# Performance work log

Measured on AMD Instinct MI355X. Metric: run time of the kernel, lower is better.

Reference implementation:

```python
import jax, jax.numpy as jnp
import numpy as np

B, LQ, E = 4, 8400, 256
HEADS, LEVELS, POINTS = 8, 4, 4
HEAD_DIM = E // HEADS
SHAPES = [(80, 80), (40, 40), (20, 20), (10, 10)]  # (H, W) per level; sum HW = 8400
LV = sum(h * w for h, w in SHAPES)


def setup_inputs() -> dict:
    key = jax.random.key(0)
    ks = jax.random.split(key, 12)
    query = jax.random.normal(ks[0], (B, LQ, E), jnp.float32)
    # per-level normalized reference points in (0.1, 0.9)
    reference_points = 0.1 + 0.8 * jax.random.uniform(ks[1], (B, LQ, LEVELS, 2), jnp.float32)
    value = jax.random.normal(ks[2], (B, LV, E), jnp.float32)
    spatial_shapes = jnp.array(SHAPES, dtype=jnp.int32)
    s = 0.05
    Wv = jax.random.normal(ks[3], (E, E), jnp.float32) * s
    bv = jnp.zeros((E,), jnp.float32)
    Woff = jax.random.normal(ks[4], (E, HEADS * LEVELS * POINTS * 2), jnp.float32) * 0.01
    boff = jax.random.normal(ks[5], (HEADS * LEVELS * POINTS * 2,), jnp.float32) * 0.02
    Wattn = jax.random.normal(ks[6], (E, HEADS * LEVELS * POINTS), jnp.float32) * s
    battn = jnp.zeros((HEADS * LEVELS * POINTS,), jnp.float32)
    Wo = jax.random.normal(ks[7], (E, E), jnp.float32) * s
    bo = jnp.zeros((E,), jnp.float32)
    return dict(query=query, reference_points=reference_points, value=value,
                spatial_shapes=spatial_shapes, Wv=Wv, bv=bv, Woff=Woff, boff=boff,
                Wattn=Wattn, battn=battn, Wo=Wo, bo=bo)


def _bilinear_sample(vflat, x, y, Hl, Wl):
    # vflat: [BH, D, Hl*Wl]; x, y: [BH, N] pixel coords (align_corners=False convention)
    x0f = jnp.floor(x); y0f = jnp.floor(y)
    wx = (x - x0f)[:, None, :]; wy = (y - y0f)[:, None, :]
    x0 = x0f.astype(jnp.int32); y0 = y0f.astype(jnp.int32)

    def gather(ix, iy):
        valid = ((ix >= 0) & (ix < Wl) & (iy >= 0) & (iy < Hl)).astype(vflat.dtype)
        idx = jnp.clip(iy, 0, Hl - 1) * Wl + jnp.clip(ix, 0, Wl - 1)
        g = jnp.take_along_axis(vflat, idx[:, None, :], axis=2)  # [BH, D, N]
        return g * valid[:, None, :]

    v00 = gather(x0, y0); v01 = gather(x0 + 1, y0)
    v10 = gather(x0, y0 + 1); v11 = gather(x0 + 1, y0 + 1)
    return (v00 * (1 - wx) * (1 - wy) + v01 * wx * (1 - wy)
            + v10 * (1 - wx) * wy + v11 * wx * wy)


def _msda_forward(query, reference_points, value, spatial_shapes,
                  Wv, bv, Woff, boff, Wattn, battn, Wo, bo):
    b, lq, _ = query.shape
    v = (value @ Wv + bv).reshape(b, -1, HEADS, HEAD_DIM)
    off = (query @ Woff + boff).reshape(b, lq, HEADS, LEVELS, POINTS, 2)
    aw = (query @ Wattn + battn).reshape(b, lq, HEADS, LEVELS * POINTS)
    aw = jax.nn.softmax(aw, axis=-1).reshape(b, lq, HEADS, LEVELS, POINTS)
    # normalizer (W, H) per level
    norm = jnp.stack([spatial_shapes[:, 1], spatial_shapes[:, 0]], axis=-1).astype(query.dtype)
    # sampling locations in [0,1]: [B, Lq, H, L, P, 2]
    loc = reference_points[:, :, None, :, None, :] + off / norm[None, None, None, :, None, :]

    sampled_levels = []
    start = 0
    for lvl, (Hl, Wl) in enumerate(SHAPES):
        vl = v[:, start:start + Hl * Wl]                      # [B, Hl*Wl, H, D]
        start += Hl * Wl
        vflat = vl.transpose(0, 2, 3, 1).reshape(b * HEADS, HEAD_DIM, Hl * Wl)
        grid = loc[:, :, :, lvl]                              # [B, Lq, H, P, 2]
        grid = grid.transpose(0, 2, 1, 3, 4).reshape(b * HEADS, lq * POINTS, 2)
        g = grid * 2.0 - 1.0                                  # grid_sample convention
        x = (g[..., 0] + 1.0) * (Wl * 0.5) - 0.5
        y = (g[..., 1] + 1.0) * (Hl * 0.5) - 0.5
        s = _bilinear_sample(vflat, x, y, Hl, Wl)             # [BH, D, Lq*P]
        sampled_levels.append(s.reshape(b, HEADS, HEAD_DIM, lq, POINTS))
    sampled = jnp.stack(sampled_levels, axis=-1)              # [B, H, D, Lq, P, L]
    out = jnp.einsum('bhdqpl,bqhlp->bqhd', sampled, aw).reshape(b, lq, E)
    return out @ Wo + bo


def reference(query, reference_points, value, spatial_shapes,
              Wv, bv, Woff, boff, Wattn, battn, Wo, bo):
    return _msda_forward(query, reference_points, value, spatial_shapes,
                         Wv, bv, Woff, boff, Wattn, battn, Wo, bo)
```

## Files before the change

### kernel.cpp

```cpp
#include <hip/hip_runtime.h>
#include <math.h>

#define BB 4
#define LQ 8400
#define NH 8
#define LVTOT 8500
#define HD 32
#define PLANE_USH 544000

typedef __attribute__((ext_vector_type(8))) short short8;
typedef __attribute__((ext_vector_type(4))) float f32x4;
typedef __attribute__((ext_vector_type(2))) _Float16 half2_t;
typedef __attribute__((ext_vector_type(2))) __fp16 fp16x2_t;
typedef unsigned short ushort_t;

__device__ __forceinline__ ushort_t f2bf(float f) {
    union { float f; unsigned u; } v; v.f = f;
    unsigned r = v.u + 0x7fffu + ((v.u >> 16) & 1u);
    return (ushort_t)(r >> 16);
}
__device__ __forceinline__ float bflo(unsigned u) {
    union { unsigned u; float f; } x; x.u = u << 16; return x.f;
}
__device__ __forceinline__ float bfhi(unsigned u) {
    union { unsigned u; float f; } x; x.u = u & 0xffff0000u; return x.f;
}
__device__ __forceinline__ half2_t ash2(unsigned u) {
    union { unsigned u; half2_t h; } x; x.u = u; return x.h;
}
__device__ __forceinline__ unsigned pk2u(fp16x2_t h) {
    union { fp16x2_t h; unsigned u; } x; x.h = h; return x.u;
}

__device__ __forceinline__ void dma16(const ushort_t* g, ushort_t* l) {
    __builtin_amdgcn_global_load_lds(
        (const __attribute__((address_space(1))) void*)g,
        (__attribute__((address_space(3))) void*)l, 16, 0, 0);
}

__device__ __forceinline__ void lvl_decomp(int pix, int& lb, int& y, int& x,
                                           int& rowp) {
    if (pix < 6400)      { y = pix / 80;            x = pix - y * 80;  rowp = 40; lb = 0; }
    else if (pix < 8000) { int r = pix - 6400; y = r / 40; x = r - y * 40; rowp = 20; lb = 3200; }
    else if (pix < 8400) { int r = pix - 8000; y = r / 20; x = r - y * 20; rowp = 10; lb = 4000; }
    else                 { int r = pix - 8400; y = r / 10; x = r - y * 10; rowp = 5;  lb = 4200; }
}

__global__ __launch_bounds__(256) void prep_all(
    const float* __restrict__ value, const float* __restrict__ query,
    const float* __restrict__ Wv, const float* __restrict__ Woff,
    const float* __restrict__ Wattn, const float* __restrict__ Wo,
    ushort_t* __restrict__ value_b, ushort_t* __restrict__ query_b,
    ushort_t* __restrict__ BT)
{
    const int bid = blockIdx.x;
    if (bid < 16900) {
        const float* src = (bid < 8500) ? value : query;
        ushort_t* dst = (bid < 8500) ? value_b : query_b;
        int i = (bid < 8500 ? bid : bid - 8500) * 256 + threadIdx.x;
        float4 f = ((const float4*)src)[i];
        ushort4 o;
        o.x = f2bf(f.x); o.y = f2bf(f.y); o.z = f2bf(f.z); o.w = f2bf(f.w);
        ((ushort4*)dst)[i] = o;
    } else {
        int idx = (bid - 16900) * 256 + threadIdx.x;
        int r = idx >> 8, k = idx & 255;
        float v;
        if (r < 256) v = Wv[k * 256 + r];
        else if (r < 640) {
            int n = r - 256;
            v = (n < 256) ? Woff[k * 256 + n] : Wattn[k * 128 + (n - 256)];
        } else v = Wo[k * 256 + (r - 640)];
        BT[idx] = f2bf(v);
    }
}

__device__ __forceinline__ void gemm_core(
    const ushort_t* __restrict__ A, const ushort_t* __restrict__ B, int M,
    int m0, int n0, ushort_t* Asl, ushort_t* Bsl, f32x4 acc[4][4])
{
    const int tid  = threadIdx.x;
    const int wave = tid >> 6, lane = tid & 63;
    const int quad = lane >> 4, mr = lane & 15;
    const int wm   = (wave >> 1) * 64, wn = (wave & 1) * 64;
    const int oct  = lane >> 3;
    const int bseg = lane & 7;

    for (int k0 = 0; k0 < 256; k0 += 64) {
        __syncthreads();
        #pragma unroll
        for (int i = 0; i < 4; i++) {
            int m  = i * 32 + wave * 8 + oct;
            int gs = bseg ^ (m & 7);
            int am = min(m0 + m, M - 1);
            dma16(A + (size_t)am * 256 + k0 + gs * 8,
                  Asl + (size_t)(i * 32 + wave * 8) * 64 + lane * 8);
            int bn = n0 + m;
            dma16(B + (size_t)bn * 256 + k0 + gs * 8,
                  Bsl + (size_t)(i * 32 + wave * 8) * 64 + lane * 8);
        }
        __syncthreads();
        #pragma unroll
        for (int ks = 0; ks < 2; ks++) {
            short8 af[4], bf[4];
            const int ksl = ks * 4 + quad;
            #pragma unroll
            for (int i = 0; i < 4; i++) {
                int m = wm + i * 16 + mr;
                af[i] = *(const short8*)&Asl[m * 64 + (ksl ^ (m & 7)) * 8];
                int n = wn + i * 16 + mr;
                bf[i] = *(const short8*)&Bsl[n * 64 + (ksl ^ (n & 7)) * 8];
            }
            #pragma unroll
            for (int i = 0; i < 4; i++)
                #pragma unroll
                for (int j = 0; j < 4; j++)
                    acc[i][j] = __builtin_amdgcn_mfma_f32_16x16x32_bf16(
                        af[i], bf[j], acc[i][j], 0, 0, 0);
        }
    }
}

__global__ __launch_bounds__(256, 3) void gemm_fused(
    const ushort_t* __restrict__ Av, const ushort_t* __restrict__ Aq,
    const ushort_t* __restrict__ BT,
    const float* __restrict__ bv, const float* __restrict__ boff,
    const float* __restrict__ battn,
    ushort_t* __restrict__ vperm, ushort_t* __restrict__ off_b,
    ushort_t* __restrict__ awl_b)
{
    __shared__ ushort_t smem[16384];
    ushort_t* Asl = smem;
    ushort_t* Bsl = smem + 8192;

    const int bid = blockIdx.x;
    int mode, m0, n0, M;
    const ushort_t *A, *B;
    if (bid < 532) { mode = 0; m0 = (bid >> 1) * 128; n0 = (bid & 1) * 128;
                     A = Av; B = BT; M = 34000; }
    else { int b2 = bid - 532;
           mode = 1; m0 = (b2 / 3) * 128; n0 = (b2 % 3) * 128;
           A = Aq; B = BT + 65536; M = 33600; }

    f32x4 acc[4][4];
    #pragma unroll
    for (int i = 0; i < 4; i++)
        #pragma unroll
        for (int j = 0; j < 4; j++) acc[i][j] = (f32x4){0.f, 0.f, 0.f, 0.f};

    gemm_core(A, B, M, m0, n0, Asl, Bsl, acc);

    const int tid  = threadIdx.x;
    const int wave = tid >> 6, lane = tid & 63;
    const int quad = lane >> 4, mr = lane & 15;
    const int wm   = (wave >> 1) * 64, wn = (wave & 1) * 64;

    __syncthreads();
    #pragma unroll
    for (int i = 0; i < 4; i++) {
        #pragma unroll
        for (int j = 0; j < 4; j++) {
            const int lc = wn + j * 16 + mr;
            const int c  = n0 + lc;
            const float bias = (mode == 0) ? bv[c]
                              : (c < 256 ? boff[c] : battn[c - 256]);
            #pragma unroll
            for (int reg = 0; reg < 4; reg++) {
                const int rl = wm + i * 16 + quad * 4 + reg;
                float val = acc[i][j][reg] + bias;
                ushort_t u;
                if (mode == 0) { union { _Float16 h; ushort_t u; } cv;
                                 cv.h = (_Float16)val; u = cv.u; }
                else u = f2bf(val);
                smem[rl * 128 + (lc ^ ((rl & 3) << 3))] = u;
            }
        }
    }
    __syncthreads();

    if (mode == 1) {
        for (int k = 0; k < 8; k++) {
            int sid = k * 256 + tid;
            int rl = sid >> 4, cc = (sid & 15) * 8;
            int row = m0 + rl;
            if (row >= M) continue;
            uint4 v = *(const uint4*)&smem[rl * 128 + (cc ^ ((rl & 3) << 3))];
            if (n0 < 256) *(uint4*)&off_b[(size_t)row * 256 + n0 + cc] = v;
            else          *(uint4*)&awl_b[(size_t)row * 128 + cc] = v;
        }
    } else {
        const int hb = n0 >> 5;
        for (int k = 0; k < 16; k++) {
            int sid = k * 256 + tid;
            int unit = sid >> 5;
            if (unit >= 127) continue;
            int sub = sid & 31;
            int hh = sub >> 3, q = sub & 7;
            int copy = (unit >= 64) ? 1 : 0;
            int t = copy ? ((unit - 64) * 2 + 1) : (unit * 2);
            int row = m0 + t;
            if (row + 1 >= 34000) continue;
            int b = row / LVTOT, pix = row - b * LVTOT;
            int lb, y, x, rowp;
            lvl_decomp(pix, lb, y, x, rowp);
            if (copy && x >= 2 * rowp - 1) continue;
            int p = x >> 1;
            int pidx = copy * 4250 + lb + y * rowp + p;
            int h = hb + hh;
            uint2 a  = *(const uint2*)&smem[t * 128 +
                          ((hh * 32 + q * 4) ^ ((t & 3) << 3))];
            uint2 b2 = *(const uint2*)&smem[(t + 1) * 128 +
                          ((hh * 32 + q * 4) ^ (((t + 1) & 3) << 3))];
            uint4 o;
            o.x = (a.x & 0xffffu) | (b2.x << 16);
            o.y = (a.x >> 16)     | (b2.x & 0xffff0000u);
            o.z = (a.y & 0xffffu) | (b2.y << 16);
            o.w = (a.y >> 16)     | (b2.y & 0xffff0000u);
            *(uint4*)((char*)(vperm + (size_t)(b * NH + h) * PLANE_USH)
                      + (size_t)pidx * 128 + q * 16) = o;
        }
        {
            int pixsel = tid >> 7;
            int rem = tid & 127;
            int hh = rem >> 5, d = rem & 31;
            int t = pixsel ? 127 : 0;
            int row = m0 + t;
            if (row < 34000) {
                int b = row / LVTOT, pix = row - b * LVTOT;
                int lb, y, x, rowp;
                lvl_decomp(pix, lb, y, x, rowp);
                bool doit; int p, slot;
                if (!pixsel) { doit = (x >= 2);            p = (x - 2) >> 1; slot = 1; }
                else         { doit = (x < 2 * rowp - 1);  p = (x - 1) >> 1; slot = 0; }
                if (doit) {
                    int pidx = 4250 + lb + y * rowp + p;
                    int h = hb + hh;
                    vperm[(size_t)(b * NH + h) * PLANE_USH
                          + (size_t)pidx * 64 + d * 2 + slot] =
                        smem[t * 128 + ((hh * 32 + d) ^ ((t & 3) << 3))];
                }
            }
        }
    }
}

__global__ __launch_bounds__(256, 3) void gemm_out(
    const ushort_t* __restrict__ A, const ushort_t* __restrict__ BT,
    const float* __restrict__ bo, float* __restrict__ out)
{
    __shared__ ushort_t Asl[128 * 64];
    __shared__ ushort_t Bsl[128 * 64];

    const int m0 = (blockIdx.x >> 1) * 128;
    const int n0 = (blockIdx.x & 1) * 128;
    const int M = 33600;

    f32x4 acc[4][4];
    #pragma unroll
    for (int i = 0; i < 4; i++)
        #pragma unroll
        for (int j = 0; j < 4; j++) acc[i][j] = (f32x4){0.f, 0.f, 0.f, 0.f};

    gemm_core(A, BT, M, m0, n0, Asl, Bsl, acc);

    const int tid  = threadIdx.x;
    const int wave = tid >> 6, lane = tid & 63;
    const int quad = lane >> 4, mr = lane & 15;
    const int wm   = (wave >> 1) * 64, wn = (wave & 1) * 64;

    #pragma unroll
    for (int i = 0; i < 4; i++) {
        const int rbase = m0 + wm + i * 16 + quad * 4;
        #pragma unroll
        for (int j = 0; j < 4; j++) {
            const int c = n0 + wn + j * 16 + mr;
            #pragma unroll
            for (int reg = 0; reg < 4; reg++) {
                int row = rbase + reg;
                if (row >= M) continue;
                out[(size_t)row * 256 + c] = acc[i][j][reg] + bo[c];
            }
        }
    }
}

__global__ __launch_bounds__(256) void msda_sample(
    const ushort_t* __restrict__ vperm, const ushort_t* __restrict__ off,
    const ushort_t* __restrict__ awl, const float* __restrict__ refp,
    ushort_t* __restrict__ sampled)
{
    __shared__ int4 s_wi[16 * 33];

    const int tid = threadIdx.x;
    const int bid = blockIdx.x;
    const int h   = bid & 7;
    const int r   = bid >> 3;
    const int b   = r / 263;
    const int c   = r - b * 263;
    const int q0b = c * 32;
    const size_t bq0 = (size_t)b * LQ + q0b;

    const int Hs[4]    = {80, 40, 20, 10};
    const int pbase[4] = {0, 3200, 4000, 4200};

    #pragma unroll
    for (int it = 0; it < 2; it++) {
        const int s  = it * 256 + tid;
        const int ql = s >> 4, lp = s & 15;
        const int l  = lp >> 2;
        const int qv = (q0b + ql < LQ) ? ql : 0;
        const size_t bq = bq0 + qv;
        const int Wl = Hs[l];

        unsigned od = *(const unsigned*)(off + bq * 256 + h * 32 + lp * 2);
        float ox = bflo(od), oy = bfhi(od);
        float lgt = bflo((unsigned)awl[bq * 128 + h * 16 + lp]);
        float e = __expf(lgt);
        float sum = e;
        sum += __shfl_xor(sum, 1, 16);
        sum += __shfl_xor(sum, 2, 16);
        sum += __shfl_xor(sum, 4, 16);
        sum += __shfl_xor(sum, 8, 16);
        float aw = e * __builtin_amdgcn_rcpf(sum);

        float2 rp = *(const float2*)(refp + bq * 8 + l * 2);
        float x = rp.x * (float)Wl + ox - 0.5f;
        float y = rp.y * (float)Wl + oy - 0.5f;
        float x0f = floorf(x), y0f = floorf(y);
        float wx = x - x0f, wy = y - y0f;
        int x0 = (int)x0f, y0 = (int)y0f;
        float hx0 = ((x0 >= 0) & (x0 < Wl)) ? (1.f - wx) : 0.f;
        float hx1 = ((x0 + 1 >= 0) & (x0 + 1 < Wl)) ? wx : 0.f;
        float vy0w = ((y0 >= 0) & (y0 < Wl)) ? (1.f - wy) * aw : 0.f;
        float vy1w = ((y0 + 1 >= 0) & (y0 + 1 < Wl)) ? wy * aw : 0.f;
        int px = min(max(x0, 0), Wl - 2);
        float pl, pr;
        if (x0 < px)      { pl = hx1; pr = 0.f; }
        else if (x0 > px) { pl = 0.f; pr = hx0; }
        else              { pl = hx0; pr = hx1; }
        int cy0 = min(max(y0, 0), Wl - 1);
        int cy1 = min(max(y0 + 1, 0), Wl - 1);
        const int copy = px & 1;
        const int p    = copy ? ((px - 1) >> 1) : (px >> 1);
        const int rowp = Wl >> 1;
        const int cb   = copy * 4250 + pbase[l] + p;
        const int otop = (cb + cy0 * rowp) << 7;
        const int obot = (cb + cy1 * rowp) << 7;
        unsigned wt = pk2u(__builtin_amdgcn_cvt_pkrtz(pl * vy0w, pr * vy0w));
        unsigned wb = pk2u(__builtin_amdgcn_cvt_pkrtz(pl * vy1w, pr * vy1w));
        s_wi[lp * 33 + ql] = make_int4((int)wt, (int)wb, otop, obot);
    }
    __syncthreads();

    const int ql  = tid >> 3;
    const int l8  = tid & 7;
    const int dby = l8 * 16;

    if (q0b + ql < LQ) {
        const char* plane = (const char*)(vperm + (size_t)(b * NH + h) * PLANE_USH);
        float a0 = 0.f, a1 = 0.f, a2 = 0.f, a3 = 0.f;
        #pragma unroll
        for (int pt = 0; pt < 16; pt++) {
            int4 wi = s_wi[pt * 33 + ql];
            uint4 vt = *(const uint4*)(plane + (unsigned)(wi.z + dby));
            uint4 vb = *(const uint4*)(plane + (unsigned)(wi.w + dby));
            half2_t wt = ash2((unsigned)wi.x);
            half2_t wb = ash2((unsigned)wi.y);
            a0 = __builtin_amdgcn_fdot2(wt, ash2(vt.x), a0, false);
            a0 = __builtin_amdgcn_fdot2(wb, ash2(vb.x), a0, false);
            a1 = __builtin_amdgcn_fdot2(wt, ash2(vt.y), a1, false);
            a1 = __builtin_amdgcn_fdot2(wb, ash2(vb.y), a1, false);
            a2 = __builtin_amdgcn_fdot2(wt, ash2(vt.z), a2, false);
            a2 = __builtin_amdgcn_fdot2(wb, ash2(vb.z), a2, false);
            a3 = __builtin_amdgcn_fdot2(wt, ash2(vt.w), a3, false);
            a3 = __builtin_amdgcn_fdot2(wb, ash2(vb.w), a3, false);
        }
        const size_t bq = bq0 + ql;
        ushort4 o;
        o.x = f2bf(a0); o.y = f2bf(a1);
        o.z = f2bf(a2); o.w = f2bf(a3);
        *(ushort4*)(sampled + bq * 256 + h * 32 + l8 * 4) = o;
    }
}

extern "C" void kernel_launch(void* const* d_in, const int* in_sizes, int n_in,
                              void* d_out, int out_size, void* d_ws, size_t ws_size,
                              hipStream_t stream) {
    const float* query = (const float*)d_in[0];
    const float* refp  = (const float*)d_in[1];
    const float* value = (const float*)d_in[2];
    const float* Wv    = (const float*)d_in[4];
    const float* bv    = (const float*)d_in[5];
    const float* Woff  = (const float*)d_in[6];
    const float* boff  = (const float*)d_in[7];
    const float* Wattn = (const float*)d_in[8];
    const float* battn = (const float*)d_in[9];
    const float* Wo    = (const float*)d_in[10];
    const float* bo    = (const float*)d_in[11];
    float* out = (float*)d_out;

    ushort_t* ws = (ushort_t*)d_ws;
    ushort_t* off_b   = ws;
    ushort_t* awl_b   = off_b + 8601600;
    ushort_t* value_b = awl_b + 4300800;
    ushort_t* query_b = value_b + 8704000;
    ushort_t* vperm_b = query_b + 8601600;
    ushort_t* BT      = vperm_b + 17408000;
    ushort_t* sampled_b = query_b;

    prep_all<<<dim3(17796), 256, 0, stream>>>(
        value, query, Wv, Woff, Wattn, Wo, value_b, query_b, BT);

    gemm_fused<<<dim3(532 + 789), 256, 0, stream>>>(
        value_b, query_b, BT, bv, boff, battn, vperm_b, off_b, awl_b);

    msda_sample<<<dim3(8 * 4 * 263), 256, 0, stream>>>(
        vperm_b, off_b, awl_b, refp, sampled_b);

    gemm_out<<<dim3(526), 256, 0, stream>>>(
        sampled_b, BT + 163840, bo, out);
}
```

Before: 217.8 us.

## Enlarge GEMM tiles to 256x128 with 512-thread blocks

```diff
diff --git a/kernel.cpp b/kernel.cpp
--- a/kernel.cpp
+++ b/kernel.cpp
@@ -75,7 +75,7 @@
     }
 }
 
-__device__ __forceinline__ void gemm_core(
+__device__ __forceinline__ void gemm_core256(
     const ushort_t* __restrict__ A, const ushort_t* __restrict__ B, int M,
     int m0, int n0, ushort_t* Asl, ushort_t* Bsl, f32x4 acc[4][4])
 {
@@ -90,14 +90,19 @@
         __syncthreads();
         #pragma unroll
         for (int i = 0; i < 4; i++) {
-            int m  = i * 32 + wave * 8 + oct;
+            int m  = i * 64 + wave * 8 + oct;
             int gs = bseg ^ (m & 7);
             int am = min(m0 + m, M - 1);
             dma16(A + (size_t)am * 256 + k0 + gs * 8,
-                  Asl + (size_t)(i * 32 + wave * 8) * 64 + lane * 8);
-            int bn = n0 + m;
+                  Asl + (i * 64 + wave * 8) * 64 + lane * 8);
+        }
+        #pragma unroll
+        for (int i = 0; i < 2; i++) {
+            int n  = i * 64 + wave * 8 + oct;
+            int gs = bseg ^ (n & 7);
+            int bn = n0 + n;
             dma16(B + (size_t)bn * 256 + k0 + gs * 8,
-                  Bsl + (size_t)(i * 32 + wave * 8) * 64 + lane * 8);
+                  Bsl + (i * 64 + wave * 8) * 64 + lane * 8);
         }
         __syncthreads();
         #pragma unroll
@@ -121,7 +126,7 @@
     }
 }
 
-__global__ __launch_bounds__(256, 3) void gemm_fused(
+__global__ __launch_bounds__(512, 4) void gemm_fused(
     const ushort_t* __restrict__ Av, const ushort_t* __restrict__ Aq,
     const ushort_t* __restrict__ BT,
     const float* __restrict__ bv, const float* __restrict__ boff,
@@ -129,17 +134,17 @@
     ushort_t* __restrict__ vperm, ushort_t* __restrict__ off_b,
     ushort_t* __restrict__ awl_b)
 {
-    __shared__ ushort_t smem[16384];
+    __shared__ ushort_t smem[24576];
     ushort_t* Asl = smem;
-    ushort_t* Bsl = smem + 8192;
+    ushort_t* Bsl = smem + 16384;
 
     const int bid = blockIdx.x;
     int mode, m0, n0, M;
     const ushort_t *A, *B;
-    if (bid < 532) { mode = 0; m0 = (bid >> 1) * 128; n0 = (bid & 1) * 128;
+    if (bid < 266) { mode = 0; m0 = (bid >> 1) * 256; n0 = (bid & 1) * 128;
                      A = Av; B = BT; M = 34000; }
-    else { int b2 = bid - 532;
-           mode = 1; m0 = (b2 / 3) * 128; n0 = (b2 % 3) * 128;
+    else { int b2 = bid - 266;
+           mode = 1; m0 = (b2 / 3) * 256; n0 = (b2 % 3) * 128;
            A = Aq; B = BT + 65536; M = 33600; }
 
     f32x4 acc[4][4];
@@ -148,110 +153,120 @@
         #pragma unroll
         for (int j = 0; j < 4; j++) acc[i][j] = (f32x4){0.f, 0.f, 0.f, 0.f};
 
-    gemm_core(A, B, M, m0, n0, Asl, Bsl, acc);
+    gemm_core256(A, B, M, m0, n0, Asl, Bsl, acc);
 
     const int tid  = threadIdx.x;
     const int wave = tid >> 6, lane = tid & 63;
     const int quad = lane >> 4, mr = lane & 15;
     const int wm   = (wave >> 1) * 64, wn = (wave & 1) * 64;
+    const int whalf = wave >> 2;
 
     __syncthreads();
-    #pragma unroll
-    for (int i = 0; i < 4; i++) {
-        #pragma unroll
-        for (int j = 0; j < 4; j++) {
-            const int lc = wn + j * 16 + mr;
-            const int c  = n0 + lc;
-            const float bias = (mode == 0) ? bv[c]
-                              : (c < 256 ? boff[c] : battn[c - 256]);
-            #pragma unroll
-            for (int reg = 0; reg < 4; reg++) {
-                const int rl = wm + i * 16 + quad * 4 + reg;
-                float val = acc[i][j][reg] + bias;
-                ushort_t u;
-                if (mode == 0) { union { _Float16 h; ushort_t u; } cv;
-                                 cv.h = (_Float16)val; u = cv.u; }
-                else u = f2bf(val);
-                smem[rl * 128 + (lc ^ ((rl & 3) << 3))] = u;
-            }
-        }
-    }
-    __syncthreads();
-
-    if (mode == 1) {
-        for (int k = 0; k < 8; k++) {
-            int sid = k * 256 + tid;
-            int rl = sid >> 4, cc = (sid & 15) * 8;
-            int row = m0 + rl;
-            if (row >= M) continue;
-            uint4 v = *(const uint4*)&smem[rl * 128 + (cc ^ ((rl & 3) << 3))];
-            if (n0 < 256) *(uint4*)&off_b[(size_t)row * 256 + n0 + cc] = v;
-            else          *(uint4*)&awl_b[(size_t)row * 128 + cc] = v;
-        }
-    } else {
-        const int hb = n0 >> 5;
-        for (int k = 0; k < 16; k++) {
-            int sid = k * 256 + tid;
-            int unit = sid >> 5;
-            if (unit >= 127) continue;
-            int sub = sid & 31;
-            int hh = sub >> 3, q = sub & 7;
-            int copy = (unit >= 64) ? 1 : 0;
-            int t = copy ? ((unit - 64) * 2 + 1) : (unit * 2);
-            int row = m0 + t;
-            if (row + 1 >= 34000) continue;
-            int b = row / LVTOT, pix = row - b * LVTOT;
-            int lb, y, x, rowp;
-            lvl_decomp(pix, lb, y, x, rowp);
-            if (copy && x >= 2 * rowp - 1) continue;
-            int p = x >> 1;
-            int pidx = copy * 4250 + lb + y * rowp + p;
-            int h = hb + hh;
-            uint2 a  = *(const uint2*)&smem[t * 128 +
-                          ((hh * 32 + q * 4) ^ ((t & 3) << 3))];
-            uint2 b2 = *(const uint2*)&smem[(t + 1) * 128 +
-                          ((hh * 32 + q * 4) ^ (((t + 1) & 3) << 3))];
-            uint4 o;
-            o.x = (a.x & 0xffffu) | (b2.x << 16);
-            o.y = (a.x >> 16)     | (b2.x & 0xffff0000u);
-            o.z = (a.y & 0xffffu) | (b2.y << 16);
-            o.w = (a.y >> 16)     | (b2.y & 0xffff0000u);
-            *(uint4*)((char*)(vperm + (size_t)(b * NH + h) * PLANE_USH)
-                      + (size_t)pidx * 128 + q * 16) = o;
-        }
-        {
-            int pixsel = tid >> 7;
-            int rem = tid & 127;
-            int hh = rem >> 5, d = rem & 31;
-            int t = pixsel ? 127 : 0;
-            int row = m0 + t;
-            if (row < 34000) {
+
+    for (int half = 0; half < 2; half++) {
+        if (whalf == half) {
+            #pragma unroll
+            for (int i = 0; i < 4; i++) {
+                #pragma unroll
+                for (int j = 0; j < 4; j++) {
+                    const int lc = wn + j * 16 + mr;
+                    const int c  = n0 + lc;
+                    const float bias = (mode == 0) ? bv[c]
+                                      : (c < 256 ? boff[c] : battn[c - 256]);
+                    #pragma unroll
+                    for (int reg = 0; reg < 4; reg++) {
+                        const int rl = (wm & 127) + i * 16 + quad * 4 + reg;
+                        float val = acc[i][j][reg] + bias;
+                        ushort_t u;
+                        if (mode == 0) { union { _Float16 h; ushort_t u; } cv;
+                                         cv.h = (_Float16)val; u = cv.u; }
+                        else u = f2bf(val);
+                        smem[rl * 128 + (lc ^ ((rl & 3) << 3))] = u;
+                    }
+                }
+            }
+        }
+        __syncthreads();
+
+        const int m0h = m0 + half * 128;
+        if (mode == 1) {
+            #pragma unroll
+            for (int k = 0; k < 4; k++) {
+                int sid = k * 512 + tid;
+                int rl = sid >> 4, cc = (sid & 15) * 8;
+                int row = m0h + rl;
+                if (row >= M) continue;
+                uint4 v = *(const uint4*)&smem[rl * 128 + (cc ^ ((rl & 3) << 3))];
+                if (n0 < 256) *(uint4*)&off_b[(size_t)row * 256 + n0 + cc] = v;
+                else          *(uint4*)&awl_b[(size_t)row * 128 + cc] = v;
+            }
+        } else {
+            const int hb = n0 >> 5;
+            #pragma unroll
+            for (int k = 0; k < 8; k++) {
+                int sid = k * 512 + tid;
+                int unit = sid >> 5;
+                if (unit >= 127) continue;
+                int sub = sid & 31;
+                int hh = sub >> 3, q = sub & 7;
+                int copy = (unit >= 64) ? 1 : 0;
+                int t = copy ? ((unit - 64) * 2 + 1) : (unit * 2);
+                int row = m0h + t;
+                if (row + 1 >= 34000) continue;
                 int b = row / LVTOT, pix = row - b * LVTOT;
                 int lb, y, x, rowp;
                 lvl_decomp(pix, lb, y, x, rowp);
-                bool doit; int p, slot;
-                if (!pixsel) { doit = (x >= 2);            p = (x - 2) >> 1; slot = 1; }
-                else         { doit = (x < 2 * rowp - 1);  p = (x - 1) >> 1; slot = 0; }
-                if (doit) {
-                    int pidx = 4250 + lb + y * rowp + p;
-                    int h = hb + hh;
-                    vperm[(size_t)(b * NH + h) * PLANE_USH
-                          + (size_t)pidx * 64 + d * 2 + slot] =
-                        smem[t * 128 + ((hh * 32 + d) ^ ((t & 3) << 3))];
+                if (copy && x >= 2 * rowp - 1) continue;
+                int p = x >> 1;
+                int pidx = copy * 4250 + lb + y * rowp + p;
+                int h = hb + hh;
+                uint2 a  = *(const uint2*)&smem[t * 128 +
+                              ((hh * 32 + q * 4) ^ ((t & 3) << 3))];
+                uint2 b2 = *(const uint2*)&smem[(t + 1) * 128 +
+                              ((hh * 32 + q * 4) ^ (((t + 1) & 3) << 3))];
+                uint4 o;
+                o.x = (a.x & 0xffffu) | (b2.x << 16);
+                o.y = (a.x >> 16)     | (b2.x & 0xffff0000u);
+                o.z = (a.y & 0xffffu) | (b2.y << 16);
+                o.w = (a.y >> 16)     | (b2.y & 0xffff0000u);
+                *(uint4*)((char*)(vperm + (size_t)(b * NH + h) * PLANE_USH)
+                          + (size_t)pidx * 128 + q * 16) = o;
+            }
+            if (tid < 256) {
+                int pixsel = tid >> 7;
+                int rem = tid & 127;
+                int hh = rem >> 5, d = rem & 31;
+                int t = pixsel ? 127 : 0;
+                int row = m0h + t;
+                if (row < 34000) {
+                    int b = row / LVTOT, pix = row - b * LVTOT;
+                    int lb, y, x, rowp;
+                    lvl_decomp(pix, lb, y, x, rowp);
+                    bool doit; int p, slot;
+                    if (!pixsel) { doit = (x >= 2);            p = (x - 2) >> 1; slot = 1; }
+                    else         { doit = (x < 2 * rowp - 1);  p = (x - 1) >> 1; slot = 0; }
+                    if (doit) {
+                        int pidx = 4250 + lb + y * rowp + p;
+                        int h = hb + hh;
+                        vperm[(size_t)(b * NH + h) * PLANE_USH
+                              + (size_t)pidx * 64 + d * 2 + slot] =
+                            smem[t * 128 + ((hh * 32 + d) ^ ((t & 3) << 3))];
+                    }
                 }
             }
         }
-    }
-}
-
-__global__ __launch_bounds__(256, 3) void gemm_out(
+        __syncthreads();
+    }
+}
+
+__global__ __launch_bounds__(512, 4) void gemm_out(
     const ushort_t* __restrict__ A, const ushort_t* __restrict__ BT,
     const float* __restrict__ bo, float* __restrict__ out)
 {
-    __shared__ ushort_t Asl[128 * 64];
+    __shared__ ushort_t Asl[256 * 64];
     __shared__ ushort_t Bsl[128 * 64];
 
-    const int m0 = (blockIdx.x >> 1) * 128;
+    const int m0 = (blockIdx.x >> 1) * 256;
     const int n0 = (blockIdx.x & 1) * 128;
     const int M = 33600;
 
@@ -261,7 +276,7 @@
         #pragma unroll
         for (int j = 0; j < 4; j++) acc[i][j] = (f32x4){0.f, 0.f, 0.f, 0.f};
 
-    gemm_core(A, BT, M, m0, n0, Asl, Bsl, acc);
+    gemm_core256(A, BT, M, m0, n0, Asl, Bsl, acc);
 
     const int tid  = threadIdx.x;
     const int wave = tid >> 6, lane = tid & 63;
@@ -411,12 +426,12 @@
     prep_all<<<dim3(17796), 256, 0, stream>>>(
         value, query, Wv, Woff, Wattn, Wo, value_b, query_b, BT);
 
-    gemm_fused<<<dim3(532 + 789), 256, 0, stream>>>(
+    gemm_fused<<<dim3(266 + 396), 512, 0, stream>>>(
         value_b, query_b, BT, bv, boff, battn, vperm_b, off_b, awl_b);
 
     msda_sample<<<dim3(8 * 4 * 263), 256, 0, stream>>>(
         vperm_b, off_b, awl_b, refp, sampled_b);
 
-    gemm_out<<<dim3(526), 256, 0, stream>>>(
+    gemm_out<<<dim3(264), 512, 0, stream>>>(
         sampled_b, BT + 163840, bo, out);
 }
```

Measured after the change: 262.9 us. +20.7%, slower.
